# Kernel tuning notes

Measured on AMD Instinct MI355X. Metric: run time of the kernel, lower is better.

## Reference

```python
import jax, jax.numpy as jnp
import numpy as np

N_NODES = 100000


def _gcn_edges(edge_index, num_nodes):
    # Add self-loops and compute symmetric GCN normalization per edge.
    src = jnp.concatenate([edge_index[0], jnp.arange(num_nodes, dtype=edge_index.dtype)])
    dst = jnp.concatenate([edge_index[1], jnp.arange(num_nodes, dtype=edge_index.dtype)])
    deg = jnp.zeros((num_nodes,), jnp.float32).at[dst].add(1.0)
    dinv = jnp.where(deg > 0, jax.lax.rsqrt(deg), 0.0)
    norm = dinv[src] * dinv[dst]  # [E+N]
    return src, dst, norm


def _gcn_conv(x, W, b, src, dst, norm, num_nodes):
    h = x @ W                         # [N, d_out] transform first (d_out <= d_in)
    msg = h[src] * norm[:, None]      # [E, d_out] gather + scale
    agg = jax.ops.segment_sum(msg, dst, num_segments=num_nodes)
    return agg + b


def setup_inputs() -> dict:
    key = jax.random.key(0)
    k = jax.random.split(key, 8)
    n, e, d_in, d_out = N_NODES, 1600000, 128, 64
    hid = 2 * d_out
    s = lambda fan: 1.0 / np.sqrt(fan)
    return {
        "x": jax.random.normal(k[0], (n, d_in), jnp.float32),
        "edge_index": jax.random.randint(k[1], (2, e), 0, n, jnp.int64),
        "W1": jax.random.normal(k[2], (d_in, hid), jnp.float32) * s(d_in),
        "b1": jnp.zeros((hid,), jnp.float32),
        "Wmu": jax.random.normal(k[3], (hid, d_out), jnp.float32) * s(hid),
        "bmu": jnp.zeros((d_out,), jnp.float32),
        "Wls": jax.random.normal(k[4], (hid, d_out), jnp.float32) * s(hid),
        "bls": jnp.zeros((d_out,), jnp.float32),
    }


def reference(x, edge_index, W1, b1, Wmu, bmu, Wls, bls):
    n = x.shape[0]
    src, dst, norm = _gcn_edges(edge_index, n)
    h = jax.nn.relu(_gcn_conv(x, W1, b1, src, dst, norm, n))
    mu = _gcn_conv(h, Wmu, bmu, src, dst, norm, n)
    logstd = _gcn_conv(h, Wls, bls, src, dst, norm, n)
    return mu, logstd
```

## Files before the change

kernel.cpp:

```cpp
#include <hip/hip_runtime.h>

#define DIN 128
#define HID 128
#define DOUT 64
#define NCHUNK 784
#define CHB 8
#define BSH 9
#define NB1MAX 256
#define BSLACK 1540
#define EBMAX 16384

typedef unsigned short ushort_t;
typedef unsigned int uint_t;
typedef __attribute__((ext_vector_type(4))) short s4v;
typedef __attribute__((ext_vector_type(4))) float f4v;

#if defined(__has_builtin)
#if __has_builtin(__builtin_amdgcn_mfma_f32_16x16x16bf16_1k)
#define MFMA16(a, b, c) __builtin_amdgcn_mfma_f32_16x16x16bf16_1k(a, b, c, 0, 0, 0)
#endif
#endif
#ifndef MFMA16
static __device__ inline f4v mfma16_asm(s4v a, s4v b, f4v c) {
  asm volatile("v_mfma_f32_16x16x16_bf16 %0, %1, %2, %0" : "+v"(c) : "v"(a), "v"(b));
  return c;
}
#define MFMA16(a, b, c) mfma16_asm(a, b, c)
#endif

static inline int ceil_div(int a, int b) { return (a + b - 1) / b; }

__device__ inline ushort_t f2bf(float f) {
  uint_t u = __float_as_uint(f);
  u += 0x7fff + ((u >> 16) & 1);
  return (ushort_t)(u >> 16);
}
__device__ inline uint_t pack2bf(float a, float b) {
  return (uint_t)f2bf(a) | ((uint_t)f2bf(b) << 16);
}
__device__ inline float2 bf2x2(uint_t u) {
  return make_float2(__uint_as_float(u << 16), __uint_as_float(u & 0xffff0000u));
}

__device__ inline int blk_scan_incl(int v, int* ws, int nw) {
  int t = threadIdx.x, lane = t & 63, w = t >> 6;
#pragma unroll
  for (int d = 1; d < 64; d <<= 1) {
    int u = __shfl_up(v, d, 64);
    if (lane >= d) v += u;
  }
  if (lane == 63) ws[w] = v;
  __syncthreads();
  if (w == 0) {
    int s = (lane < nw) ? ws[lane] : 0;
    for (int d = 1; d < nw; d <<= 1) {
      int u = __shfl_up(s, d, 64);
      if (lane >= d) s += u;
    }
    if (lane < nw) ws[lane] = s;
  }
  __syncthreads();
  if (w > 0) v += ws[w - 1];
  return v;
}


__global__ __launch_bounds__(512) void k_setup(const int* __restrict__ dst, int E, int CH,
                                               int nb1, int* __restrict__ counts,
                                               const float* __restrict__ x,
                                               const float* __restrict__ W1,
                                               const float* __restrict__ Wmu,
                                               const float* __restrict__ Wls,
                                               ushort_t* __restrict__ Wt2,
                                               ushort_t* __restrict__ xWb,
                                               ushort_t* __restrict__ h,
                                               float* __restrict__ dinv, int N, int G1) {
  __shared__ ushort_t Ws[128][132];
  __shared__ uint_t cnt[NB1MAX];
  int b = blockIdx.x, t = threadIdx.x;
  if (b < G1) {
#pragma unroll
    for (int it = 0; it < 16; it++) {
      int k = it * 8 + ((t >> 7) << 1);
      int j = t & 127;
      float a = W1[k * 128 + j];
      float bb = W1[(k + 1) * 128 + j];
      *(uint_t*)&Ws[j][k] = pack2bf(a, bb);
    }
    __syncthreads();
    int w = t >> 6, lane = t & 63;
    int rl = lane & 15, g = lane >> 4;
    int row = b * 128 + w * 16 + rl;
    bool valid = row < N;
    const float* Ar = x + (size_t)row * DIN + 4 * g;
    s4v af[8];
#pragma unroll
    for (int kk = 0; kk < 8; kk++) {
      float4 v = make_float4(0.f, 0.f, 0.f, 0.f);
      if (valid) v = *(const float4*)(Ar + kk * 16);
      s4v a;
      a[0] = (short)f2bf(v.x);
      a[1] = (short)f2bf(v.y);
      a[2] = (short)f2bf(v.z);
      a[3] = (short)f2bf(v.w);
      af[kk] = a;
    }
    f4v acc[8];
#pragma unroll
    for (int ct = 0; ct < 8; ct++) acc[ct] = (f4v)0.f;
#pragma unroll
    for (int kk = 0; kk < 8; kk++) {
      int ko = kk * 16 + 4 * g;
#pragma unroll
      for (int ct = 0; ct < 8; ct++) {
        s4v bb = *(s4v*)&Ws[ct * 16 + rl][ko];
        acc[ct] = MFMA16(af[kk], bb, acc[ct]);
      }
    }
    int gr0 = b * 128 + w * 16 + 4 * g;
#pragma unroll
    for (int i = 0; i < 4; i++) {
      int gr = gr0 + i;
      if (gr < N) {
#pragma unroll
        for (int ct = 0; ct < 8; ct++)
          xWb[(size_t)gr * HID + ct * 16 + rl] = f2bf(acc[ct][i]);
      }
    }
  } else if (b < G1 + NCHUNK) {
    int c = b - G1;
    for (int i = t; i < nb1; i += 512) cnt[i] = 0;
    __syncthreads();
    int e0 = c * CH, e1 = min(E, e0 + CH);
    for (int i = e0 + t; i < e1; i += 512) atomicAdd(&cnt[((uint_t)dst[i]) >> BSH], 1u);
    __syncthreads();
    for (int i = t; i < nb1; i += 512) counts[c * nb1 + i] = (int)cnt[i];
  } else if (b < G1 + NCHUNK + 32) {
    int idx = (b - G1 - NCHUNK) * 512 + t;
    int j = idx >> 7, k = idx & 127;
    Wt2[j * 128 + k] = f2bf(j < 64 ? Wmu[k * 64 + j] : Wls[k * 64 + (j - 64)]);
  } else {
    if (t < 64) ((uint_t*)(xWb + (size_t)N * HID))[t] = 0;
    else if (t < 128) ((uint_t*)(h + (size_t)N * HID))[t - 64] = 0;
    else if (t == 128) dinv[N] = 0.f;
  }
}

__global__ __launch_bounds__(256) void k_bscan(const int* __restrict__ counts, int nb1,
                                               int* __restrict__ chunk_off,
                                               int* __restrict__ btot) {
  __shared__ int ws[8];
  __shared__ int shc;
  int b = blockIdx.x, t = threadIdx.x;
  int carry = 0;
#pragma unroll
  for (int r = 0; r < NCHUNK / 256 + 1; r++) {
    int idx = r * 256 + t;
    int v = (idx < NCHUNK) ? counts[idx * nb1 + b] : 0;
    int incl = blk_scan_incl(v, ws, 4) + carry;
    if (idx < NCHUNK) chunk_off[idx * nb1 + b] = incl - v;
    if (t == 255) shc = incl;
    __syncthreads();
    carry = shc;
  }
  if (t == 0) btot[b] = carry;
}

__global__ __launch_bounds__(256) void k_bscatter(const int* __restrict__ src,
                                                  const int* __restrict__ dst, int E, int CH,
                                                  int nb1, const int* __restrict__ btot,
                                                  const int* __restrict__ chunk_off,
                                                  uint_t* __restrict__ tmp) {
  __shared__ int ws[8];
  __shared__ uint_t cnt[NB1MAX];
  __shared__ uint_t lofs[NB1MAX];
  __shared__ uint_t gbase[NB1MAX];
  __shared__ uint_t ebuf[CHB * 256];
  __shared__ ushort_t bbuf[CHB * 256];
  int t = threadIdx.x, c = blockIdx.x;
  {
    int v = (t < nb1) ? btot[t] : 0;
    int incl = blk_scan_incl(v, ws, 4);
    if (t < nb1) {
      gbase[t] = (uint_t)(incl - v + chunk_off[c * nb1 + t]);
      cnt[t] = 0;
    }
  }
  __syncthreads();
  int e0 = c * CH, e1 = min(E, e0 + CH);
  int nloc = e1 - e0;
  uint_t pay[CHB];
  ushort_t bk[CHB], rk[CHB];
#pragma unroll
  for (int r = 0; r < CHB; r++) {
    int i = e0 + r * 256 + t;
    if (i < e1) {
      uint_t d = (uint_t)dst[i];
      uint_t s = (uint_t)src[i];
      uint_t b = d >> BSH;
      pay[r] = ((d & ((1u << BSH) - 1)) << 17) | s;
      bk[r] = (ushort_t)b;
      rk[r] = (ushort_t)atomicAdd(&cnt[b], 1u);
    }
  }
  __syncthreads();
  {
    int v = (t < nb1) ? (int)cnt[t] : 0;
    int incl = blk_scan_incl(v, ws, 4);
    if (t < nb1) lofs[t] = (uint_t)(incl - v);
  }
  __syncthreads();
#pragma unroll
  for (int r = 0; r < CHB; r++) {
    int i = e0 + r * 256 + t;
    if (i < e1) {
      uint_t p = lofs[bk[r]] + rk[r];
      ebuf[p] = pay[r];
      bbuf[p] = bk[r];
    }
  }
  __syncthreads();
  for (int i = t; i < nloc; i += 256) {
    uint_t b = bbuf[i];
    tmp[gbase[b] + ((uint_t)i - lofs[b])] = ebuf[i];
  }
}

__global__ __launch_bounds__(512) void k_bfinal(const uint_t* __restrict__ tmp,
                                                const int* __restrict__ btot, int N, int nb1,
                                                uint_t* __restrict__ csr,
                                                int* __restrict__ row_ptr,
                                                int* __restrict__ row_end,
                                                float* __restrict__ dinv) {
  __shared__ int ws[8];
  __shared__ int sseg0, sseg1, sptot;
  __shared__ uint_t cnt[1 << BSH];
  __shared__ uint_t ppfx[1 << BSH];
  __shared__ uint_t cur[1 << BSH];
  __shared__ uint_t ebuf[EBMAX];
  int b = blockIdx.x, t = threadIdx.x;
  {
    int v = (t < nb1) ? btot[t] : 0;
    int incl = blk_scan_incl(v, ws, 8);
    if (t == b) {
      sseg0 = incl - v;
      sseg1 = incl;
    }
  }
  for (int i = t; i < (1 << BSH); i += 512) cnt[i] = 0;
  __syncthreads();
  int seg0 = sseg0, seg1 = sseg1;
  int pb = ((seg0 + 3) & ~3) + BSLACK * b;
  for (int i = seg0 + t; i < seg1; i += 512) atomicAdd(&cnt[tmp[i] >> 17], 1u);
  __syncthreads();
  if (t < 64) {
    uint_t pc[8];
    uint_t s = 0;
#pragma unroll
    for (int k = 0; k < 8; k++) {
      pc[k] = (cnt[t * 8 + k] + 3u) & ~3u;
      s += pc[k];
    }
    int incl = (int)s;
#pragma unroll
    for (int d = 1; d < 64; d <<= 1) {
      int u = __shfl_up(incl, d, 64);
      if (t >= d) incl += u;
    }
    uint_t excl = (uint_t)incl - s;
#pragma unroll
    for (int k = 0; k < 8; k++) {
      ppfx[t * 8 + k] = excl;
      excl += pc[k];
    }
    if (t == 63) sptot = (int)excl;
  }
  __syncthreads();
  int ptot = sptot;
  int nd0 = b << BSH;
  for (int i = t; i < (1 << BSH); i += 512) {
    cur[i] = ppfx[i];
    int g = nd0 + i;
    if (g < N) {
      row_ptr[g] = pb + (int)ppfx[i];
      row_end[g] = pb + (int)(ppfx[i] + ((cnt[i] + 3u) & ~3u));
      dinv[g] = rsqrtf((float)cnt[i] + 1.0f);
    }
  }
  for (int i = t; i < ptot; i += 512) ebuf[i] = (uint_t)N;
  __syncthreads();
  for (int i = seg0 + t; i < seg1; i += 512) {
    uint_t v = tmp[i];
    uint_t pos = atomicAdd(&cur[v >> 17], 1u);
    ebuf[pos] = v & 0x1FFFFu;
  }
  __syncthreads();
  for (int i = t; i < ptot; i += 512) csr[pb + i] = ebuf[i];
}


__global__ __launch_bounds__(256) void k_agg1(const ushort_t* __restrict__ H,
                                              const int* __restrict__ row_ptr,
                                              const int* __restrict__ row_end,
                                              const uint_t* __restrict__ csr,
                                              const float* __restrict__ dinv,
                                              const float* __restrict__ bias,
                                              ushort_t* __restrict__ out, int n) {
  int node = (blockIdx.x * blockDim.x + threadIdx.x) >> 6;
  int lane = threadIdx.x & 63;
  if (node >= n) return;
  const char* Hb = (const char*)H;
  const char* Db = (const char*)dinv;
  uint_t loff = (uint_t)lane << 2;
  float dn = dinv[node];
  int j = row_ptr[node], end = row_end[node];
  float2 hs = bf2x2(*(const uint_t*)(Hb + ((size_t)(((uint_t)node << 8) | loff))));
  float ax = dn * hs.x, ay = dn * hs.y;
  if (j < end) {
    uint4 c = *(const uint4*)(csr + j);
    while (true) {
      int jn = j + 4;
      bool more = jn < end;
      uint4 cn;
      if (more) cn = *(const uint4*)(csr + jn);
      float w0 = *(const float*)(Db + (size_t)(c.x << 2));
      float w1 = *(const float*)(Db + (size_t)(c.y << 2));
      float w2 = *(const float*)(Db + (size_t)(c.z << 2));
      float w3 = *(const float*)(Db + (size_t)(c.w << 2));
      uint_t v0 = *(const uint_t*)(Hb + (size_t)((c.x << 8) | loff));
      uint_t v1 = *(const uint_t*)(Hb + (size_t)((c.y << 8) | loff));
      uint_t v2 = *(const uint_t*)(Hb + (size_t)((c.z << 8) | loff));
      uint_t v3 = *(const uint_t*)(Hb + (size_t)((c.w << 8) | loff));
      float2 f0 = bf2x2(v0), f1 = bf2x2(v1), f2 = bf2x2(v2), f3 = bf2x2(v3);
      ax += w0 * f0.x; ay += w0 * f0.y;
      ax += w1 * f1.x; ay += w1 * f1.y;
      ax += w2 * f2.x; ay += w2 * f2.y;
      ax += w3 * f3.x; ay += w3 * f3.y;
      if (!more) break;
      c = cn;
      j = jn;
    }
  }
  ax = fmaxf(dn * ax + bias[2 * lane], 0.f) * dn;
  ay = fmaxf(dn * ay + bias[2 * lane + 1], 0.f) * dn;
  ((uint_t*)out)[(size_t)node * 64 + lane] = pack2bf(ax, ay);
}


__global__ __launch_bounds__(256) void k_agg2(const ushort_t* __restrict__ H,
                                              const int* __restrict__ row_ptr,
                                              const int* __restrict__ row_end,
                                              const uint_t* __restrict__ csr,
                                              const float* __restrict__ dinv,
                                              ushort_t* __restrict__ out, int n) {
  int node = (blockIdx.x * blockDim.x + threadIdx.x) >> 6;
  int lane = threadIdx.x & 63;
  if (node >= n) return;
  const char* Hb = (const char*)H;
  uint_t loff = (uint_t)lane << 2;
  float dn = dinv[node];
  int j = row_ptr[node], end = row_end[node];
  float2 hs = bf2x2(*(const uint_t*)(Hb + ((size_t)(((uint_t)node << 8) | loff))));
  float ax = hs.x, ay = hs.y;
  if (j < end) {
    uint4 c = *(const uint4*)(csr + j);
    while (true) {
      int jn = j + 4;
      bool more = jn < end;
      uint4 cn;
      if (more) cn = *(const uint4*)(csr + jn);
      uint_t v0 = *(const uint_t*)(Hb + (size_t)((c.x << 8) | loff));
      uint_t v1 = *(const uint_t*)(Hb + (size_t)((c.y << 8) | loff));
      uint_t v2 = *(const uint_t*)(Hb + (size_t)((c.z << 8) | loff));
      uint_t v3 = *(const uint_t*)(Hb + (size_t)((c.w << 8) | loff));
      float2 f0 = bf2x2(v0), f1 = bf2x2(v1), f2 = bf2x2(v2), f3 = bf2x2(v3);
      ax += f0.x + f1.x;
      ay += f0.y + f1.y;
      ax += f2.x + f3.x;
      ay += f2.y + f3.y;
      if (!more) break;
      c = cn;
      j = jn;
    }
  }
  ax *= dn;
  ay *= dn;
  ((uint_t*)out)[(size_t)node * 64 + lane] = pack2bf(ax, ay);
}


__global__ __launch_bounds__(256) void k_gemm2(const ushort_t* __restrict__ A,
                                               const ushort_t* __restrict__ Wt,
                                               const float* __restrict__ bmu,
                                               const float* __restrict__ bls,
                                               float* __restrict__ out, int n) {
  __shared__ ushort_t Ws[128][132];
  int t = threadIdx.x;
#pragma unroll
  for (int i = 0; i < 16; i++) {
    int f = t + 256 * i;
    int rowj = f >> 5, seg = f & 31;
    *(uint2*)&Ws[rowj][seg * 4] = *(const uint2*)(Wt + rowj * 128 + seg * 4);
  }
  __syncthreads();
  int w = t >> 6, lane = t & 63;
  int rl = lane & 15, g = lane >> 4;
  int row = blockIdx.x * 64 + w * 16 + rl;
  bool valid = row < n;
  const ushort_t* Ar = A + (size_t)row * HID + 4 * g;
  s4v af[8];
#pragma unroll
  for (int kk = 0; kk < 8; kk++) {
    s4v a = (s4v)0;
    if (valid) a = *(const s4v*)(Ar + kk * 16);
    af[kk] = a;
  }
  f4v acc[8];
#pragma unroll
  for (int ct = 0; ct < 8; ct++) acc[ct] = (f4v)0.f;
#pragma unroll
  for (int kk = 0; kk < 8; kk++) {
    int ko = kk * 16 + 4 * g;
#pragma unroll
    for (int ct = 0; ct < 8; ct++) {
      s4v b = *(s4v*)&Ws[ct * 16 + rl][ko];
      acc[ct] = MFMA16(af[kk], b, acc[ct]);
    }
  }
  int gr0 = blockIdx.x * 64 + w * 16 + 4 * g;
#pragma unroll
  for (int ct = 0; ct < 8; ct++) {
    int col = ct * 16 + rl;
    float bv;
    size_t obase;
    int cc;
    if (ct < 4) {
      bv = bmu[col];
      obase = 0;
      cc = col;
    } else {
      bv = bls[col - 64];
      obase = (size_t)n * DOUT;
      cc = col - 64;
    }
#pragma unroll
    for (int i = 0; i < 4; i++) {
      int gr = gr0 + i;
      if (gr < n) out[obase + (size_t)gr * DOUT + cc] = acc[ct][i] + bv;
    }
  }
}


extern "C" void kernel_launch(void* const* d_in, const int* in_sizes, int n_in,
                              void* d_out, int out_size, void* d_ws, size_t ws_size,
                              hipStream_t stream) {
  const float* x   = (const float*)d_in[0];
  const int*   ei  = (const int*)d_in[1];
  const float* W1  = (const float*)d_in[2];
  const float* b1  = (const float*)d_in[3];
  const float* Wmu = (const float*)d_in[4];
  const float* bmu = (const float*)d_in[5];
  const float* Wls = (const float*)d_in[6];
  const float* bls = (const float*)d_in[7];
  float* out = (float*)d_out;

  const int N = in_sizes[0] / DIN;
  const int E = in_sizes[1] / 2;
  const int* esrc = ei;
  const int* edst = ei + E;
  const int nb1 = ceil_div(N, 1 << BSH);
  const int CH = ceil_div(E, NCHUNK);
  const int G1 = ceil_div(N, 128);

  char* ws = (char*)d_ws;
  size_t off = 0;
  auto alloc = [&](size_t bytes) -> void* {
    void* p = ws + off;
    off = (off + bytes + 255) & ~(size_t)255;
    return p;
  };
  ushort_t* xWb   = (ushort_t*)alloc((size_t)(N + 1) * HID * sizeof(ushort_t));
  ushort_t* h     = (ushort_t*)alloc((size_t)(N + 1) * HID * sizeof(ushort_t));
  uint_t* csr     = (uint_t*)alloc(((size_t)E + (size_t)(BSLACK + 8) * nb1 + 16) * 4);
  uint_t* tmp     = (uint_t*)alloc((size_t)E * 4);
  int* counts     = (int*)alloc((size_t)NCHUNK * nb1 * 4);
  int* chunk_off  = (int*)alloc((size_t)NCHUNK * nb1 * 4);
  int* btot       = (int*)alloc((size_t)nb1 * 4);
  int* row_ptr    = (int*)alloc((size_t)N * 4);
  int* row_end    = (int*)alloc((size_t)N * 4);
  float* dinv     = (float*)alloc((size_t)(N + 1) * 4);
  ushort_t* wt2b  = (ushort_t*)alloc((size_t)HID * HID * 2);
  (void)ws_size; (void)n_in; (void)out_size;

  k_setup<<<G1 + NCHUNK + 33, 512, 0, stream>>>(edst, E, CH, nb1, counts, x, W1, Wmu, Wls,
                                                wt2b, xWb, h, dinv, N, G1);
  k_bscan<<<nb1, 256, 0, stream>>>(counts, nb1, chunk_off, btot);
  k_bscatter<<<NCHUNK, 256, 0, stream>>>(esrc, edst, E, CH, nb1, btot, chunk_off, tmp);
  k_bfinal<<<nb1, 512, 0, stream>>>(tmp, btot, N, nb1, csr, row_ptr, row_end, dinv);

  k_agg1<<<ceil_div(N, 4), 256, 0, stream>>>(xWb, row_ptr, row_end, csr, dinv, b1, h, N);

  k_agg2<<<ceil_div(N, 4), 256, 0, stream>>>(h, row_ptr, row_end, csr, dinv, xWb, N);
  k_gemm2<<<ceil_div(N, 64), 256, 0, stream>>>(xWb, wt2b, bmu, bls, out, N);
}
```

Before: 205.4 us.

## Fuse layer-2 aggregation with the mu/logstd MFMA GEMM via shared-memory rows

Merges the second-layer neighbor aggregation and the output GEMM into one kernel. Each wave aggregates 16 nodes one at a time, stages the bf16 rows in LDS, then runs MFMA against W2 read straight from global memory. This drops the intermediate aggregated-feature round trip through global memory and one kernel launch. The cost is far less parallelism in the gather phase: one wave now handles 16 nodes in sequence instead of one each, with 16x fewer blocks, and W2 is read from global/L2 per wave instead of from LDS.

```diff
diff --git a/kernel.cpp b/kernel.cpp
--- a/kernel.cpp
+++ b/kernel.cpp
@@ -347,89 +347,68 @@
 }
 
 
-__global__ __launch_bounds__(256) void k_agg2(const ushort_t* __restrict__ H,
-                                              const int* __restrict__ row_ptr,
-                                              const int* __restrict__ row_end,
-                                              const uint_t* __restrict__ csr,
-                                              const float* __restrict__ dinv,
-                                              ushort_t* __restrict__ out, int n) {
-  int node = (blockIdx.x * blockDim.x + threadIdx.x) >> 6;
-  int lane = threadIdx.x & 63;
-  if (node >= n) return;
-  const char* Hb = (const char*)H;
-  uint_t loff = (uint_t)lane << 2;
-  float dn = dinv[node];
-  int j = row_ptr[node], end = row_end[node];
-  float2 hs = bf2x2(*(const uint_t*)(Hb + ((size_t)(((uint_t)node << 8) | loff))));
-  float ax = hs.x, ay = hs.y;
-  if (j < end) {
-    uint4 c = *(const uint4*)(csr + j);
-    while (true) {
-      int jn = j + 4;
-      bool more = jn < end;
-      uint4 cn;
-      if (more) cn = *(const uint4*)(csr + jn);
-      uint_t v0 = *(const uint_t*)(Hb + (size_t)((c.x << 8) | loff));
-      uint_t v1 = *(const uint_t*)(Hb + (size_t)((c.y << 8) | loff));
-      uint_t v2 = *(const uint_t*)(Hb + (size_t)((c.z << 8) | loff));
-      uint_t v3 = *(const uint_t*)(Hb + (size_t)((c.w << 8) | loff));
-      float2 f0 = bf2x2(v0), f1 = bf2x2(v1), f2 = bf2x2(v2), f3 = bf2x2(v3);
-      ax += f0.x + f1.x;
-      ay += f0.y + f1.y;
-      ax += f2.x + f3.x;
-      ay += f2.y + f3.y;
-      if (!more) break;
-      c = cn;
-      j = jn;
-    }
-  }
-  ax *= dn;
-  ay *= dn;
-  ((uint_t*)out)[(size_t)node * 64 + lane] = pack2bf(ax, ay);
-}
-
-
-__global__ __launch_bounds__(256) void k_gemm2(const ushort_t* __restrict__ A,
-                                               const ushort_t* __restrict__ Wt,
+__global__ __launch_bounds__(256) void k_agg2g(const ushort_t* __restrict__ H,
+                                               const int* __restrict__ row_ptr,
+                                               const int* __restrict__ row_end,
+                                               const uint_t* __restrict__ csr,
+                                               const float* __restrict__ dinv,
+                                               const ushort_t* __restrict__ Wt2,
                                                const float* __restrict__ bmu,
                                                const float* __restrict__ bls,
                                                float* __restrict__ out, int n) {
-  __shared__ ushort_t Ws[128][132];
-  int t = threadIdx.x;
-#pragma unroll
-  for (int i = 0; i < 16; i++) {
-    int f = t + 256 * i;
-    int rowj = f >> 5, seg = f & 31;
-    *(uint2*)&Ws[rowj][seg * 4] = *(const uint2*)(Wt + rowj * 128 + seg * 4);
-  }
-  __syncthreads();
-  int w = t >> 6, lane = t & 63;
+  __shared__ ushort_t rows[4][16][132];
+  int t = threadIdx.x, w = t >> 6, lane = t & 63;
+  int nbase = blockIdx.x * 64 + w * 16;
+  const char* Hb = (const char*)H;
+  uint_t loff = (uint_t)lane << 2;
+  for (int r = 0; r < 16; r++) {
+    int node = nbase + r;
+    float ax = 0.f, ay = 0.f;
+    if (node < n) {
+      float dn = dinv[node];
+      int j = row_ptr[node], end = row_end[node];
+      float2 hs = bf2x2(*(const uint_t*)(Hb + ((size_t)(((uint_t)node << 8) | loff))));
+      ax = hs.x;
+      ay = hs.y;
+      if (j < end) {
+        uint4 c = *(const uint4*)(csr + j);
+        while (true) {
+          int jn = j + 4;
+          bool more = jn < end;
+          uint4 cn;
+          if (more) cn = *(const uint4*)(csr + jn);
+          uint_t v0 = *(const uint_t*)(Hb + (size_t)((c.x << 8) | loff));
+          uint_t v1 = *(const uint_t*)(Hb + (size_t)((c.y << 8) | loff));
+          uint_t v2 = *(const uint_t*)(Hb + (size_t)((c.z << 8) | loff));
+          uint_t v3 = *(const uint_t*)(Hb + (size_t)((c.w << 8) | loff));
+          float2 f0 = bf2x2(v0), f1 = bf2x2(v1), f2 = bf2x2(v2), f3 = bf2x2(v3);
+          ax += f0.x + f1.x;
+          ay += f0.y + f1.y;
+          ax += f2.x + f3.x;
+          ay += f2.y + f3.y;
+          if (!more) break;
+          c = cn;
+          j = jn;
+        }
+      }
+      ax *= dn;
+      ay *= dn;
+    }
+    *(uint_t*)&rows[w][r][2 * lane] = pack2bf(ax, ay);
+  }
+  __syncthreads();
   int rl = lane & 15, g = lane >> 4;
-  int row = blockIdx.x * 64 + w * 16 + rl;
-  bool valid = row < n;
-  const ushort_t* Ar = A + (size_t)row * HID + 4 * g;
   s4v af[8];
 #pragma unroll
-  for (int kk = 0; kk < 8; kk++) {
-    s4v a = (s4v)0;
-    if (valid) a = *(const s4v*)(Ar + kk * 16);
-    af[kk] = a;
-  }
-  f4v acc[8];
-#pragma unroll
-  for (int ct = 0; ct < 8; ct++) acc[ct] = (f4v)0.f;
-#pragma unroll
-  for (int kk = 0; kk < 8; kk++) {
-    int ko = kk * 16 + 4 * g;
-#pragma unroll
-    for (int ct = 0; ct < 8; ct++) {
-      s4v b = *(s4v*)&Ws[ct * 16 + rl][ko];
-      acc[ct] = MFMA16(af[kk], b, acc[ct]);
-    }
-  }
-  int gr0 = blockIdx.x * 64 + w * 16 + 4 * g;
+  for (int kk = 0; kk < 8; kk++) af[kk] = *(s4v*)&rows[w][rl][kk * 16 + 4 * g];
 #pragma unroll
   for (int ct = 0; ct < 8; ct++) {
+    f4v acc = (f4v)0.f;
+#pragma unroll
+    for (int kk = 0; kk < 8; kk++) {
+      s4v b = *(const s4v*)(Wt2 + (size_t)(ct * 16 + rl) * 128 + kk * 16 + 4 * g);
+      acc = MFMA16(af[kk], b, acc);
+    }
     int col = ct * 16 + rl;
     float bv;
     size_t obase;
@@ -445,8 +424,8 @@
     }
 #pragma unroll
     for (int i = 0; i < 4; i++) {
-      int gr = gr0 + i;
-      if (gr < n) out[obase + (size_t)gr * DOUT + cc] = acc[ct][i] + bv;
+      int nd = nbase + 4 * g + i;
+      if (nd < n) out[obase + (size_t)nd * DOUT + cc] = acc[i] + bv;
     }
   }
 }
@@ -501,6 +480,6 @@
 
   k_agg1<<<ceil_div(N, 4), 256, 0, stream>>>(xWb, row_ptr, row_end, csr, dinv, b1, h, N);
 
-  k_agg2<<<ceil_div(N, 4), 256, 0, stream>>>(h, row_ptr, row_end, csr, dinv, xWb, N);
-  k_gemm2<<<ceil_div(N, 64), 256, 0, stream>>>(xWb, wt2b, bmu, bls, out, N);
-}
+  k_agg2g<<<ceil_div(N, 64), 256, 0, stream>>>(h, row_ptr, row_end, csr, dinv, wt2b, bmu, bls,
+                                               out, N);
+}
```

New measurement: 232.9 us. 13.4% more time.
